# Kernel optimization log

Measured on AMD Instinct MI355X. Metric: run time of the kernel, lower is better.

## Reference

```python
import jax, jax.numpy as jnp
import numpy as np

N, E, ND, ED, HID = 50000, 400000, 128, 64, 128
GIN = 2 * ND + 2  # gnn1 input dim
CIN = 2 * HID + ED  # classifier input dim


def seg_mean(v, idx, n):
    s = jax.ops.segment_sum(v, idx, num_segments=n)
    cnt = jax.ops.segment_sum(jnp.ones((v.shape[0], 1), v.dtype), idx, num_segments=n)
    return s / jnp.maximum(cnt, 1.0)


def layer_norm(h, g, b):
    mu = h.mean(-1, keepdims=True)
    var = ((h - mu) ** 2).mean(-1, keepdims=True)
    return (h - mu) / jnp.sqrt(var + 1e-5) * g + b


def gatv2(h, src, dst, ea, wl, wr, we, att, bias, n, heads):
    # PyG GATv2Conv, concat=False, negative_slope=0.2, add_self_loops with fill_value='mean'
    C = wl.shape[1] // heads
    loop_attr = seg_mean(ea, dst, n)  # self-loop edge_attr = mean of incoming edge_attr
    ar = jnp.arange(n, dtype=src.dtype)
    s = jnp.concatenate([src, ar])
    d = jnp.concatenate([dst, ar])
    ea2 = jnp.concatenate([ea, loop_attr], axis=0)
    xl = (h @ wl).reshape(n, heads, C)
    xr = (h @ wr).reshape(n, heads, C)
    e = xl[s] + xr[d] + (ea2 @ we).reshape(-1, heads, C)  # [E2, H, C]
    e = jax.nn.leaky_relu(e, 0.2)
    logit = (e * att).sum(-1)  # [E2, H]
    m = jax.ops.segment_max(logit, d, num_segments=n)
    m = jnp.where(jnp.isfinite(m), m, 0.0)
    a = jnp.exp(logit - m[d])
    denom = jax.ops.segment_sum(a, d, num_segments=n)
    a = a / jnp.maximum(denom[d], 1e-16)
    out = jax.ops.segment_sum(xl[s] * a[..., None], d, num_segments=n)  # [N, H, C]
    return out.mean(axis=1) + bias


def setup_inputs() -> dict:
    key = jax.random.key(0)
    ks = jax.random.split(key, 32)
    w = lambda k, sh: jax.random.normal(k, sh, jnp.float32) * 0.05
    x = jax.random.normal(ks[0], (N, ND), jnp.float32)
    node_stats = jax.random.uniform(ks[1], (N, 2), jnp.float32)
    src = jax.random.randint(ks[2], (E,), 0, N)
    dst = (src + 1 + jax.random.randint(ks[3], (E,), 0, N - 1)) % N  # guarantees src != dst
    edge_index = jnp.stack([src, dst]).astype(jnp.int32)
    edge_attr = jax.random.normal(ks[4], (E, ED), jnp.float32)
    return {
        'x': x, 'node_stats': node_stats, 'edge_index': edge_index, 'edge_attr': edge_attr,
        'epw': w(ks[5], (ED, ND)), 'epb': jnp.zeros((ND,), jnp.float32),
        'g1wl': w(ks[6], (GIN, 2 * HID)), 'g1wr': w(ks[7], (GIN, 2 * HID)),
        'g1we': w(ks[8], (ED, 2 * HID)), 'g1att': w(ks[9], (2, HID)), 'g1b': jnp.zeros((HID,), jnp.float32),
        'n1g': jnp.ones((HID,), jnp.float32), 'n1b': jnp.zeros((HID,), jnp.float32),
        'g2wl': w(ks[10], (HID, HID)), 'g2wr': w(ks[11], (HID, HID)),
        'g2we': w(ks[12], (ED, HID)), 'g2att': w(ks[13], (1, HID)), 'g2b': jnp.zeros((HID,), jnp.float32),
        'n2g': jnp.ones((HID,), jnp.float32), 'n2b': jnp.zeros((HID,), jnp.float32),
        'c1w': w(ks[14], (CIN, HID)), 'c1b': jnp.zeros((HID,), jnp.float32),
        'c2w': w(ks[15], (HID, HID // 2)), 'c2b': jnp.zeros((HID // 2,), jnp.float32),
        'c3w': w(ks[16], (HID // 2, 1)), 'c3b': jnp.zeros((1,), jnp.float32),
    }


def reference(x, node_stats, edge_index, edge_attr, epw, epb, g1wl, g1wr, g1we, g1att, g1b,
              n1g, n1b, g2wl, g2wr, g2we, g2att, g2b, n2g, n2b, c1w, c1b, c2w, c2b, c3w, c3b):
    src, dst = edge_index[0], edge_index[1]
    n = x.shape[0]
    emb = jax.nn.relu(edge_attr @ epw + epb)  # [E, ND]
    x_out = seg_mean(emb, src, n)
    x_in = seg_mean(emb, dst, n)
    xi = jnp.concatenate([x_out, x_in, node_stats], axis=1)  # [N, GIN]
    h1 = jax.nn.elu(layer_norm(gatv2(xi, src, dst, edge_attr, g1wl, g1wr, g1we, g1att, g1b, n, 2), n1g, n1b))
    h2 = jax.nn.elu(layer_norm(gatv2(h1, src, dst, edge_attr, g2wl, g2wr, g2we, g2att, g2b, n, 1), n2g, n2b))
    er = jnp.concatenate([h2[src], h2[dst], edge_attr], axis=1)  # [E, CIN]
    h = jax.nn.relu(er @ c1w + c1b)
    h = jax.nn.relu(h @ c2w + c2b)
    return h @ c3w + c3b  # [E, 1]
```

## Files before the change

kernel.cpp:

```cpp
#include <hip/hip_runtime.h>
#include <cstdint>
#include <cstddef>


static inline int cdiv(int a, int b) { return (a + b - 1) / b; }

typedef __attribute__((ext_vector_type(8))) short bfrag;
typedef __attribute__((ext_vector_type(4))) float ffrag;

__device__ __forceinline__ float bf2f(unsigned short u) {
  return __uint_as_float(((unsigned)u) << 16);
}
__device__ __forceinline__ unsigned short f2bf(float f) {
  unsigned b = __float_as_uint(f);
  return (unsigned short)((b + 0x7FFFu + ((b >> 16) & 1u)) >> 16);
}

struct PrepJobs {
  const float* src[11];
  unsigned short* dst[11];
  int K[11], Nc[11], KC[11], ld[11];
};
__global__ void prep_bt(PrepJobs J) {
  int j = blockIdx.x;
  int K = J.K[j], Nc = J.Nc[j], KC = J.KC[j], ld = J.ld[j];
  const float* S = J.src[j];
  unsigned short* D = J.dst[j];
  for (int n = blockIdx.y; n < Nc; n += gridDim.y)
    for (int t = threadIdx.x; t < KC; t += blockDim.x) {
      float v = (t < K) ? S[(size_t)t * ld + n] : 0.f;
      D[(size_t)n * KC + t] = f2bf(v);
    }
}

__global__ __launch_bounds__(256) void cvt_bf16(const float* __restrict__ in,
                                                unsigned short* __restrict__ out,
                                                int n4) {
  for (int i = blockIdx.x * blockDim.x + threadIdx.x; i < n4;
       i += gridDim.x * blockDim.x) {
    float4 v = ((const float4*)in)[i];
    ((ushort4*)out)[i] = make_ushort4(f2bf(v.x), f2bf(v.y), f2bf(v.z), f2bf(v.w));
  }
}

__global__ void count_deg(const int* __restrict__ src, const int* __restrict__ dst,
                          int* __restrict__ dsrc, int* __restrict__ ddst, int E) {
  int t = blockIdx.x * blockDim.x + threadIdx.x;
  if (t < E) {
    atomicAdd(&dsrc[src[t]], 1);
    atomicAdd(&ddst[dst[t]], 1);
  }
}

__global__ __launch_bounds__(256) void scan_local(
    const int* __restrict__ degA, const int* __restrict__ degB,
    int* __restrict__ rowA, int* __restrict__ rowB, int* __restrict__ bsum,
    int N, int nb) {
  __shared__ int s[256];
  int arr = blockIdx.y;
  const int* deg = arr ? degB : degA;
  int* row = arr ? rowB : rowA;
  int b = blockIdx.x;
  int i = b * 256 + threadIdx.x;
  int v = (i < N) ? deg[i] : 0;
  s[threadIdx.x] = v;
  __syncthreads();
  for (int off = 1; off < 256; off <<= 1) {
    int t = (threadIdx.x >= off) ? s[threadIdx.x - off] : 0;
    __syncthreads();
    s[threadIdx.x] += t;
    __syncthreads();
  }
  int incl = s[threadIdx.x];
  if (i < N) row[i] = incl - v;
  if (threadIdx.x == 255) bsum[arr * nb + b] = incl;
}

__global__ __launch_bounds__(1024) void scan_bsums(int* __restrict__ bsum, int nb,
                                                   int* __restrict__ rowA,
                                                   int* __restrict__ rowB, int N) {
  __shared__ int s[1024];
  int tid = threadIdx.x;
  for (int arr = 0; arr < 2; arr++) {
    int v = (tid < nb) ? bsum[arr * nb + tid] : 0;
    s[tid] = v;
    __syncthreads();
    for (int off = 1; off < 1024; off <<= 1) {
      int t = (tid >= off) ? s[tid - off] : 0;
      __syncthreads();
      s[tid] += t;
      __syncthreads();
    }
    if (tid < nb) bsum[arr * nb + tid] = s[tid] - v;
    if (tid == nb - 1) {
      int* row = arr ? rowB : rowA;
      row[N] = s[tid];
    }
    __syncthreads();
  }
}

__global__ void scan_add(int* __restrict__ rowA, int* __restrict__ rowB,
                         int* __restrict__ curA, const int* __restrict__ bsum,
                         int N, int nb) {
  int arr = blockIdx.y;
  int* row = arr ? rowB : rowA;
  int b = blockIdx.x;
  int i = b * 256 + threadIdx.x;
  if (i < N) {
    int v = row[i] + bsum[arr * nb + b];
    row[i] = v;
    if (arr == 0) curA[i] = v;
  }
}

__global__ void ext_fix(const int* __restrict__ row_dst, int* __restrict__ row_ext,
                        int* __restrict__ cur_ext, int* __restrict__ ext_eid,
                        int E, int N) {
  int i = blockIdx.x * blockDim.x + threadIdx.x;
  if (i <= N) row_ext[i] = row_dst[i] + i;
  if (i < N) {
    cur_ext[i] = row_dst[i] + i;
    ext_eid[row_dst[i + 1] + i] = E + i;
  }
}

__global__ void scatter_eid(const int* __restrict__ src, const int* __restrict__ dst,
                            int* __restrict__ csrc, int* __restrict__ cext,
                            int* __restrict__ esrc, int* __restrict__ ext_eid,
                            int E) {
  int t = blockIdx.x * blockDim.x + threadIdx.x;
  if (t < E) {
    int p = atomicAdd(&csrc[src[t]], 1);
    esrc[p] = t;
    int q = atomicAdd(&cext[dst[t]], 1);
    ext_eid[q] = t;
  }
}

struct ASrc {
  const float *p0, *p1, *p2;
  int ld0, ld1, ld2, k0, k1;
};
__device__ __forceinline__ float loadA(const ASrc& a, int m, int k) {
  if (k < a.k0) return a.p0[(size_t)m * a.ld0 + k];
  if (k < a.k1) return a.p1[(size_t)m * a.ld1 + (k - a.k0)];
  return a.p2[(size_t)m * a.ld2 + (k - a.k1)];
}
__device__ __forceinline__ int regionOf(const ASrc& a, int k) {
  return k < a.k0 ? 0 : (k < a.k1 ? 1 : 2);
}

template <int ABF>
__device__ __forceinline__ void stageA(
    const ASrc& A, const unsigned short* __restrict__ Abf, int lda,
    unsigned short* asb, int m0, int kc, int M, int K, int tid) {
  int row = tid & 63, kq = tid >> 6;
  int gm = m0 + row;
  if (ABF) {
    const unsigned short* rp = Abf + (size_t)gm * lda + kc + kq * 16;
    ushort4 z = make_ushort4(0, 0, 0, 0);
#pragma unroll
    for (int q = 0; q < 4; q++) {
      ushort4 v = (gm < M) ? *(const ushort4*)(rp + q * 4) : z;
      *(ushort4*)&asb[row * 72 + kq * 16 + q * 4] = v;
    }
  } else {
    bool fastc = (kc + 64 <= K) && (regionOf(A, kc) == regionOf(A, kc + 63)) &&
                 (gm < M);
    if (fastc) {
      int r = regionOf(A, kc);
      const float* p;
      int ld, koff;
      if (r == 0) { p = A.p0; ld = A.ld0; koff = 0; }
      else if (r == 1) { p = A.p1; ld = A.ld1; koff = A.k0; }
      else { p = A.p2; ld = A.ld2; koff = A.k1; }
      const float* rp = p + (size_t)gm * ld + (kc - koff) + kq * 16;
#pragma unroll
      for (int q = 0; q < 4; q++) {
        float4 v = *(const float4*)(rp + q * 4);
        *(ushort4*)&asb[row * 72 + kq * 16 + q * 4] =
            make_ushort4(f2bf(v.x), f2bf(v.y), f2bf(v.z), f2bf(v.w));
      }
    } else {
#pragma unroll
      for (int q = 0; q < 16; q++) {
        int kk = kc + kq * 16 + q;
        float v = (gm < M && kk < K) ? loadA(A, gm, kk) : 0.f;
        asb[row * 72 + kq * 16 + q] = f2bf(v);
      }
    }
  }
}

template <int ACT, int OBF, int ABF>
__global__ __launch_bounds__(256) void gemm_mfma(
    ASrc A, const unsigned short* __restrict__ Abf, int lda,
    const unsigned short* __restrict__ Bt, int ldbt,
    const float* __restrict__ bias, void* __restrict__ Cv, int ldc, int M, int K) {
  __shared__ __align__(16) unsigned short asb[64 * 72];
  __shared__ __align__(16) unsigned short bsb[128 * 72];
  int tid = threadIdx.x;
  int m0 = blockIdx.x * 64, n0 = blockIdx.y * 128;
  int lane = tid & 63, wave = tid >> 6;
  int quad = lane >> 4, l16 = lane & 15;
  ffrag zero = {0.f, 0.f, 0.f, 0.f};
  ffrag acc[8];
#pragma unroll
  for (int t = 0; t < 8; t++) acc[t] = zero;
  int KC = (K + 63) & ~63;
  for (int kc = 0; kc < KC; kc += 64) {
    __syncthreads();
    stageA<ABF>(A, Abf, lda, asb, m0, kc, M, K, tid);
    {
      int n = tid >> 1, hf = tid & 1;
      const ushort4* rp = (const ushort4*)(Bt + (size_t)(n0 + n) * ldbt + kc + hf * 32);
      ushort4* dp = (ushort4*)&bsb[n * 72 + hf * 32];
#pragma unroll
      for (int i = 0; i < 8; i++) dp[i] = rp[i];
    }
    __syncthreads();
    int arow = wave * 16 + l16;
    bfrag a0 = *(const bfrag*)&asb[arow * 72 + quad * 8];
    bfrag a1 = *(const bfrag*)&asb[arow * 72 + 32 + quad * 8];
#pragma unroll
    for (int t = 0; t < 8; t++) {
      int bn = t * 16 + l16;
      bfrag b0 = *(const bfrag*)&bsb[bn * 72 + quad * 8];
      bfrag b1 = *(const bfrag*)&bsb[bn * 72 + 32 + quad * 8];
      acc[t] = __builtin_amdgcn_mfma_f32_16x16x32_bf16(a0, b0, acc[t], 0, 0, 0);
      acc[t] = __builtin_amdgcn_mfma_f32_16x16x32_bf16(a1, b1, acc[t], 0, 0, 0);
    }
  }
#pragma unroll
  for (int t = 0; t < 8; t++) {
    int col = n0 + t * 16 + l16;
    float bv = bias ? bias[col] : 0.f;
#pragma unroll
    for (int r = 0; r < 4; r++) {
      int row = m0 + wave * 16 + quad * 4 + r;
      if (row < M) {
        float v = acc[t][r] + bv;
        if (ACT == 1) v = fmaxf(v, 0.f);
        if (OBF)
          ((unsigned short*)Cv)[(size_t)row * ldc + col] = f2bf(v);
        else
          ((float*)Cv)[(size_t)row * ldc + col] = v;
      }
    }
  }
}

template <int OBF, int ABF>
__global__ __launch_bounds__(256) void gemm_dual(
    ASrc A, const unsigned short* __restrict__ Abf, int lda,
    const unsigned short* __restrict__ Bt1, const unsigned short* __restrict__ Bt2,
    int ldbt, void* __restrict__ Cv1, void* __restrict__ Cv2, int ldc,
    int M, int K) {
  __shared__ __align__(16) unsigned short asb[64 * 72];
  __shared__ __align__(16) unsigned short bsb[128 * 72];
  int tid = threadIdx.x;
  int m0 = blockIdx.x * 64, n0 = blockIdx.y * 128;
  int lane = tid & 63, wave = tid >> 6;
  int quad = lane >> 4, l16 = lane & 15;
  ffrag zero = {0.f, 0.f, 0.f, 0.f};
  ffrag acc1[8], acc2[8];
#pragma unroll
  for (int t = 0; t < 8; t++) { acc1[t] = zero; acc2[t] = zero; }
  int KC = (K + 63) & ~63;
  int arow = wave * 16 + l16;
  for (int kc = 0; kc < KC; kc += 64) {
    __syncthreads();
    stageA<ABF>(A, Abf, lda, asb, m0, kc, M, K, tid);
    {
      int n = tid >> 1, hf = tid & 1;
      const ushort4* rp = (const ushort4*)(Bt1 + (size_t)(n0 + n) * ldbt + kc + hf * 32);
      ushort4* dp = (ushort4*)&bsb[n * 72 + hf * 32];
#pragma unroll
      for (int i = 0; i < 8; i++) dp[i] = rp[i];
    }
    __syncthreads();
    bfrag a0 = *(const bfrag*)&asb[arow * 72 + quad * 8];
    bfrag a1 = *(const bfrag*)&asb[arow * 72 + 32 + quad * 8];
#pragma unroll
    for (int t = 0; t < 8; t++) {
      int bn = t * 16 + l16;
      bfrag b0 = *(const bfrag*)&bsb[bn * 72 + quad * 8];
      bfrag b1 = *(const bfrag*)&bsb[bn * 72 + 32 + quad * 8];
      acc1[t] = __builtin_amdgcn_mfma_f32_16x16x32_bf16(a0, b0, acc1[t], 0, 0, 0);
      acc1[t] = __builtin_amdgcn_mfma_f32_16x16x32_bf16(a1, b1, acc1[t], 0, 0, 0);
    }
    __syncthreads();
    {
      int n = tid >> 1, hf = tid & 1;
      const ushort4* rp = (const ushort4*)(Bt2 + (size_t)(n0 + n) * ldbt + kc + hf * 32);
      ushort4* dp = (ushort4*)&bsb[n * 72 + hf * 32];
#pragma unroll
      for (int i = 0; i < 8; i++) dp[i] = rp[i];
    }
    __syncthreads();
#pragma unroll
    for (int t = 0; t < 8; t++) {
      int bn = t * 16 + l16;
      bfrag b0 = *(const bfrag*)&bsb[bn * 72 + quad * 8];
      bfrag b1 = *(const bfrag*)&bsb[bn * 72 + 32 + quad * 8];
      acc2[t] = __builtin_amdgcn_mfma_f32_16x16x32_bf16(a0, b0, acc2[t], 0, 0, 0);
      acc2[t] = __builtin_amdgcn_mfma_f32_16x16x32_bf16(a1, b1, acc2[t], 0, 0, 0);
    }
  }
#pragma unroll
  for (int t = 0; t < 8; t++) {
    int col = n0 + t * 16 + l16;
#pragma unroll
    for (int r = 0; r < 4; r++) {
      int row = m0 + wave * 16 + quad * 4 + r;
      if (row < M) {
        if (OBF) {
          ((unsigned short*)Cv1)[(size_t)row * ldc + col] = f2bf(acc1[t][r]);
          ((unsigned short*)Cv2)[(size_t)row * ldc + col] = f2bf(acc2[t][r]);
        } else {
          ((float*)Cv1)[(size_t)row * ldc + col] = acc1[t][r];
          ((float*)Cv2)[(size_t)row * ldc + col] = acc2[t][r];
        }
      }
    }
  }
}

__global__ __launch_bounds__(256) void gather_mean(
    const int* __restrict__ row_src, const int* __restrict__ eid_src,
    const int* __restrict__ row_ext, const int* __restrict__ ext_eid,
    const unsigned short* __restrict__ emb, const unsigned short* __restrict__ eab,
    float* __restrict__ xout, float* __restrict__ xin,
    unsigned short* __restrict__ lattrb, int N) {
  int lane = threadIdx.x & 63, wid = threadIdx.x >> 6;
  int n = blockIdx.x * 4 + wid;
  int side = blockIdx.y;
  if (n >= N) return;
  int lo, hi;
  const int* eid;
  if (side) { lo = row_ext[n]; hi = row_ext[n + 1] - 1; eid = ext_eid; }
  else { lo = row_src[n]; hi = row_src[n + 1]; eid = eid_src; }
  float a0 = 0.f, a1 = 0.f, la = 0.f;
  for (int j = lo; j < hi; j++) {
    int e = eid[j];
    ushort2 v = *(const ushort2*)&emb[(size_t)e * 128 + lane * 2];
    a0 += bf2f(v.x);
    a1 += bf2f(v.y);
    if (side) la += bf2f(eab[(size_t)e * 64 + lane]);
  }
  float r = 1.f / fmaxf((float)(hi - lo), 1.f);
  float* ob = side ? xin : xout;
  *(float2*)&ob[(size_t)n * 128 + lane * 2] = make_float2(a0 * r, a1 * r);
  if (side) lattrb[(size_t)n * 64 + lane] = f2bf(la * r);
}

template <int H>
__global__ __launch_bounds__(256) void attn_logits_mfma(
    const unsigned short* __restrict__ xl, const unsigned short* __restrict__ xr,
    const int* __restrict__ src, const int* __restrict__ dst,
    const unsigned short* __restrict__ eab, const unsigned short* __restrict__ lattrb,
    const int* __restrict__ ext_eid,
    const unsigned short* __restrict__ wet, const float* __restrict__ att,
    float* __restrict__ lg, int E, int N) {
  constexpr int HC = H * 128;
  __shared__ __align__(16) unsigned short asb[64 * 72];
  __shared__ __align__(16) unsigned short bsb[128 * 72];
  __shared__ float atts[128];
  __shared__ int sidx[64], didx[64];
  unsigned short* Cs = bsb;
  int tid = threadIdx.x;
  int E2 = E + N;
  int i0 = blockIdx.x * 64;
  int lane = tid & 63, wave = tid >> 6, quad = lane >> 4, l16 = lane & 15;
  if (tid < 64) {
    int j = i0 + tid;
    int s = 0, d = 0;
    if (j < E2) {
      int e = ext_eid[j];
      if (e < E) { s = src[e]; d = dst[e]; }
      else { s = d = e - E; }
    }
    sidx[tid] = s;
    didx[tid] = d;
  }
  {
    int row = tid & 63, kq = tid >> 6;
    int j = i0 + row;
    if (j < E2) {
      int e = ext_eid[j];
      const unsigned short* ap =
          (e < E) ? eab + (size_t)e * 64 : lattrb + (size_t)(e - E) * 64;
      const ushort4* rp = (const ushort4*)(ap + kq * 16);
#pragma unroll
      for (int q = 0; q < 4; q++)
        *(ushort4*)&asb[row * 72 + kq * 16 + q * 4] = rp[q];
    } else {
      ushort4 z = make_ushort4(0, 0, 0, 0);
#pragma unroll
      for (int q = 0; q < 4; q++) *(ushort4*)&asb[row * 72 + kq * 16 + q * 4] = z;
    }
  }
  int er = tid >> 4, cc = tid & 15;
  ffrag zero = {0.f, 0.f, 0.f, 0.f};
  for (int head = 0; head < H; head++) {
    int n0 = head * 128;
    __syncthreads();
    if (tid < 128) atts[tid] = att[n0 + tid];
    {
      int n = tid >> 1, hf = tid & 1;
      const ushort4* rp = (const ushort4*)(wet + (size_t)(n0 + n) * 64 + hf * 32);
      ushort4* dp = (ushort4*)&bsb[n * 72 + hf * 32];
#pragma unroll
      for (int i = 0; i < 8; i++) dp[i] = rp[i];
    }
    __syncthreads();
    int arow = wave * 16 + l16;
    bfrag a0 = *(const bfrag*)&asb[arow * 72 + quad * 8];
    bfrag a1 = *(const bfrag*)&asb[arow * 72 + 32 + quad * 8];
    ffrag acc[8];
#pragma unroll
    for (int t = 0; t < 8; t++) {
      acc[t] = zero;
      int bn = t * 16 + l16;
      bfrag b0 = *(const bfrag*)&bsb[bn * 72 + quad * 8];
      bfrag b1 = *(const bfrag*)&bsb[bn * 72 + 32 + quad * 8];
      acc[t] = __builtin_amdgcn_mfma_f32_16x16x32_bf16(a0, b0, acc[t], 0, 0, 0);
      acc[t] = __builtin_amdgcn_mfma_f32_16x16x32_bf16(a1, b1, acc[t], 0, 0, 0);
    }
    __syncthreads();
    {
      int rb = wave * 16 + quad * 4;
#pragma unroll
      for (int t = 0; t < 8; t++)
#pragma unroll
        for (int r = 0; r < 4; r++)
          Cs[(rb + r) * 136 + t * 16 + l16] = f2bf(acc[t][r]);
    }
    __syncthreads();
#pragma unroll
    for (int i2 = 0; i2 < 4; i2++) {
      int r = er * 4 + i2;
      int gi = i0 + r;
      float ps = 0.f;
      if (gi < E2) {
        int s = sidx[r], d = didx[r];
#pragma unroll
        for (int h = 0; h < 2; h++) {
          int c = h * 64 + cc * 4;
          ushort4 mv = *(const ushort4*)&Cs[r * 136 + c];
          ushort4 xlu = *(const ushort4*)&xl[(size_t)s * HC + n0 + c];
          ushort4 xru = *(const ushort4*)&xr[(size_t)d * HC + n0 + c];
          float e0 = bf2f(mv.x) + bf2f(xlu.x) + bf2f(xru.x);
          float e1 = bf2f(mv.y) + bf2f(xlu.y) + bf2f(xru.y);
          float e2 = bf2f(mv.z) + bf2f(xlu.z) + bf2f(xru.z);
          float e3 = bf2f(mv.w) + bf2f(xlu.w) + bf2f(xru.w);
          e0 = e0 > 0.f ? e0 : 0.2f * e0;
          e1 = e1 > 0.f ? e1 : 0.2f * e1;
          e2 = e2 > 0.f ? e2 : 0.2f * e2;
          e3 = e3 > 0.f ? e3 : 0.2f * e3;
          ps += e0 * atts[c + 0] + e1 * atts[c + 1] + e2 * atts[c + 2] +
                e3 * atts[c + 3];
        }
      }
      ps += __shfl_xor(ps, 1);
      ps += __shfl_xor(ps, 2);
      ps += __shfl_xor(ps, 4);
      ps += __shfl_xor(ps, 8);
      if (cc == 0 && gi < E2) lg[(size_t)gi * H + head] = ps;
    }
  }
}

template <int H>
__global__ __launch_bounds__(256) void attn_fused(
    const unsigned short* __restrict__ xl, const float* __restrict__ lg,
    const int* __restrict__ row_ext, const int* __restrict__ ext_eid,
    const int* __restrict__ src, const float* __restrict__ bias,
    const float* __restrict__ gam, const float* __restrict__ bet,
    unsigned short* __restrict__ hout, int E, int N) {
  constexpr int HC = H * 128;
  constexpr int CPL = HC / 64;
  int lane = threadIdx.x & 63, wid = threadIdx.x >> 6;
  int n = blockIdx.x * 4 + wid;
  if (n >= N) return;
  int lo = row_ext[n], hi = row_ext[n + 1];
  int myh = (H == 2) ? (lane >> 5) : 0;
  int colbase = (H == 2) ? (myh * 128 + (lane & 31) * 4) : (lane * 2);
  float m = -3.4e38f;
  for (int j = lo; j < hi; j++) m = fmaxf(m, lg[(size_t)j * H + myh]);
  float asum = 0.f;
  float acc[CPL] = {};
  for (int j = lo; j < hi; j++) {
    int e = ext_eid[j];
    int s = (e < E) ? src[e] : (e - E);
    float a = __expf(lg[(size_t)j * H + myh] - m);
    asum += a;
    const unsigned short* xp = &xl[(size_t)s * HC + colbase];
    if (H == 2) {
      ushort4 u = *(const ushort4*)xp;
      acc[0] += a * bf2f(u.x);
      acc[1] += a * bf2f(u.y);
      acc[2] += a * bf2f(u.z);
      acc[3] += a * bf2f(u.w);
    } else {
      ushort2 u = *(const ushort2*)xp;
      acc[0] += a * bf2f(u.x);
      acc[1] += a * bf2f(u.y);
    }
  }
  float inv = 1.f / fmaxf(asum, 1e-16f);
#pragma unroll
  for (int k = 0; k < CPL; k++) acc[k] *= inv;
  int ch;
  if (H == 2) {
#pragma unroll
    for (int k = 0; k < CPL; k++) acc[k] = (acc[k] + __shfl_xor(acc[k], 32)) * 0.5f;
    ch = (lane & 31) * CPL;
  } else {
    ch = lane * CPL;
  }
#pragma unroll
  for (int k = 0; k < CPL; k++) acc[k] += bias[ch + k];
  float s = 0.f;
#pragma unroll
  for (int k = 0; k < CPL; k++) s += acc[k];
#pragma unroll
  for (int mm = 1; mm < 64; mm <<= 1) s += __shfl_xor(s, mm);
  constexpr float dupn = (H == 2) ? 256.f : 128.f;
  float mu = s / dupn;
  float vs = 0.f;
#pragma unroll
  for (int k = 0; k < CPL; k++) {
    acc[k] -= mu;
    vs += acc[k] * acc[k];
  }
#pragma unroll
  for (int mm = 1; mm < 64; mm <<= 1) vs += __shfl_xor(vs, mm);
  float rstd = rsqrtf(vs / dupn + 1e-5f);
  float y[CPL];
#pragma unroll
  for (int k = 0; k < CPL; k++) {
    float v = acc[k] * rstd * gam[ch + k] + bet[ch + k];
    y[k] = v > 0.f ? v : expm1f(v);
  }
  if (H == 2) {
    if (lane < 32)
      *(ushort4*)&hout[(size_t)n * 128 + ch] =
          make_ushort4(f2bf(y[0]), f2bf(y[1]), f2bf(y[2]), f2bf(y[3]));
  } else {
    *(ushort2*)&hout[(size_t)n * 128 + ch] = make_ushort2(f2bf(y[0]), f2bf(y[1]));
  }
}

__global__ __launch_bounds__(256) void classifier_mfma(
    const unsigned short* __restrict__ eab, const unsigned short* __restrict__ Wct,
    const int* __restrict__ eid_src,
    const int* __restrict__ src, const int* __restrict__ dst,
    const float* __restrict__ P, const float* __restrict__ Q,
    const float* __restrict__ c1b, const unsigned short* __restrict__ c2t,
    const float* __restrict__ c2b, const float* __restrict__ c3w,
    const float* __restrict__ c3b, float* __restrict__ out, int E) {
  __shared__ __align__(16) unsigned short asb[64 * 72];
  __shared__ __align__(16) unsigned short bsb[128 * 72];
  __shared__ __align__(16) unsigned short t1s[64 * 136];
  __shared__ float c1bs[128];
  __shared__ float c2bs[64], c3ws[64];
  __shared__ int sidx[64], didx[64], eidx[64];
  int tid = threadIdx.x;
  int e0 = blockIdx.x * 64;
  int lane = tid & 63, wave = tid >> 6, quad = lane >> 4, l16 = lane & 15;
  if (tid < 128) c1bs[tid] = c1b[tid];
  if (tid < 64) {
    c2bs[tid] = c2b[tid];
    c3ws[tid] = c3w[tid];
    int j = e0 + tid;
    int e = (j < E) ? eid_src[j] : 0;
    eidx[tid] = (j < E) ? e : -1;
    sidx[tid] = src[e];
    didx[tid] = dst[e];
  }
  {
    int row = tid & 63, kq = tid >> 6;
    int j = e0 + row;
    if (j < E) {
      int e = eid_src[j];
      const ushort4* rp = (const ushort4*)(eab + (size_t)e * 64 + kq * 16);
#pragma unroll
      for (int q = 0; q < 4; q++)
        *(ushort4*)&asb[row * 72 + kq * 16 + q * 4] = rp[q];
    } else {
      ushort4 z = make_ushort4(0, 0, 0, 0);
#pragma unroll
      for (int q = 0; q < 4; q++) *(ushort4*)&asb[row * 72 + kq * 16 + q * 4] = z;
    }
  }
  {
    int n = tid >> 1, hf = tid & 1;
    const ushort4* rp = (const ushort4*)(Wct + (size_t)n * 64 + hf * 32);
    ushort4* dp = (ushort4*)&bsb[n * 72 + hf * 32];
#pragma unroll
    for (int i = 0; i < 8; i++) dp[i] = rp[i];
  }
  __syncthreads();
  ffrag zero = {0.f, 0.f, 0.f, 0.f};
  int arow = wave * 16 + l16;
  {
    bfrag a0 = *(const bfrag*)&asb[arow * 72 + quad * 8];
    bfrag a1 = *(const bfrag*)&asb[arow * 72 + 32 + quad * 8];
    ffrag acc[8];
#pragma unroll
    for (int t = 0; t < 8; t++) {
      acc[t] = zero;
      int bn = t * 16 + l16;
      bfrag b0 = *(const bfrag*)&bsb[bn * 72 + quad * 8];
      bfrag b1 = *(const bfrag*)&bsb[bn * 72 + 32 + quad * 8];
      acc[t] = __builtin_amdgcn_mfma_f32_16x16x32_bf16(a0, b0, acc[t], 0, 0, 0);
      acc[t] = __builtin_amdgcn_mfma_f32_16x16x32_bf16(a1, b1, acc[t], 0, 0, 0);
    }
    __syncthreads();
    int rb = wave * 16 + quad * 4;
#pragma unroll
    for (int t = 0; t < 8; t++)
#pragma unroll
      for (int r = 0; r < 4; r++)
        t1s[(rb + r) * 136 + t * 16 + l16] = f2bf(acc[t][r]);
  }
  __syncthreads();
  {
    int erow = tid >> 4, ccc = tid & 15;
#pragma unroll
    for (int i2 = 0; i2 < 4; i2++) {
      int r = erow * 4 + i2;
      int s = sidx[r], d = didx[r];
#pragma unroll
      for (int h = 0; h < 2; h++) {
        int c = h * 64 + ccc * 4;
        ushort4 mv = *(const ushort4*)&t1s[r * 136 + c];
        float4 pv = *(const float4*)&P[(size_t)s * 128 + c];
        float4 qv = *(const float4*)&Q[(size_t)d * 128 + c];
        float v0 = fmaxf(bf2f(mv.x) + pv.x + qv.x + c1bs[c + 0], 0.f);
        float v1 = fmaxf(bf2f(mv.y) + pv.y + qv.y + c1bs[c + 1], 0.f);
        float v2 = fmaxf(bf2f(mv.z) + pv.z + qv.z + c1bs[c + 2], 0.f);
        float v3 = fmaxf(bf2f(mv.w) + pv.w + qv.w + c1bs[c + 3], 0.f);
        *(ushort4*)&t1s[r * 136 + c] =
            make_ushort4(f2bf(v0), f2bf(v1), f2bf(v2), f2bf(v3));
      }
    }
    int n = tid >> 2, qq = tid & 3;
    const ushort4* rp = (const ushort4*)(c2t + (size_t)n * 128 + qq * 32);
    ushort4* dp = (ushort4*)&bsb[n * 136 + qq * 32];
#pragma unroll
    for (int i = 0; i < 8; i++) dp[i] = rp[i];
  }
  __syncthreads();
  {
    bfrag pa[4];
#pragma unroll
    for (int kc = 0; kc < 4; kc++)
      pa[kc] = *(const bfrag*)&t1s[arow * 136 + kc * 32 + quad * 8];
    ffrag acc2[4];
#pragma unroll
    for (int t = 0; t < 4; t++) {
      acc2[t] = zero;
      int bn = t * 16 + l16;
#pragma unroll
      for (int kc = 0; kc < 4; kc++) {
        bfrag b = *(const bfrag*)&bsb[bn * 136 + kc * 32 + quad * 8];
        acc2[t] = __builtin_amdgcn_mfma_f32_16x16x32_bf16(pa[kc], b, acc2[t], 0, 0, 0);
      }
    }
    float c3b0 = c3b[0];
    float rsum[4] = {0.f, 0.f, 0.f, 0.f};
#pragma unroll
    for (int t = 0; t < 4; t++) {
      int col = t * 16 + l16;
      float cb = c2bs[col], cw = c3ws[col];
#pragma unroll
      for (int r = 0; r < 4; r++)
        rsum[r] += fmaxf(acc2[t][r] + cb, 0.f) * cw;
    }
#pragma unroll
    for (int r = 0; r < 4; r++) {
      rsum[r] += __shfl_xor(rsum[r], 1);
      rsum[r] += __shfl_xor(rsum[r], 2);
      rsum[r] += __shfl_xor(rsum[r], 4);
      rsum[r] += __shfl_xor(rsum[r], 8);
    }
    if (l16 == 0) {
#pragma unroll
      for (int r = 0; r < 4; r++) {
        int e = eidx[wave * 16 + quad * 4 + r];
        if (e >= 0) out[e] = rsum[r] + c3b0;
      }
    }
  }
}

extern "C" void kernel_launch(void* const* d_in, const int* in_sizes, int n_in,
                              void* d_out, int out_size, void* d_ws, size_t ws_size,
                              hipStream_t stream) {
  const int N = in_sizes[1] / 2;
  const int E = in_sizes[3] / 64;
  const int E2 = E + N;
  const int nb = cdiv(N, 256);

  const float* node_stats = (const float*)d_in[1];
  const int* src = (const int*)d_in[2];
  const int* dst = (const int*)d_in[2] + E;
  const float* edge_attr = (const float*)d_in[3];
  const float* epw = (const float*)d_in[4];
  const float* epb = (const float*)d_in[5];
  const float* g1wl = (const float*)d_in[6];
  const float* g1wr = (const float*)d_in[7];
  const float* g1we = (const float*)d_in[8];
  const float* g1att = (const float*)d_in[9];
  const float* g1b = (const float*)d_in[10];
  const float* n1g = (const float*)d_in[11];
  const float* n1b = (const float*)d_in[12];
  const float* g2wl = (const float*)d_in[13];
  const float* g2wr = (const float*)d_in[14];
  const float* g2we = (const float*)d_in[15];
  const float* g2att = (const float*)d_in[16];
  const float* g2b = (const float*)d_in[17];
  const float* n2g = (const float*)d_in[18];
  const float* n2b = (const float*)d_in[19];
  const float* c1w = (const float*)d_in[20];
  const float* c1b = (const float*)d_in[21];
  const float* c2w = (const float*)d_in[22];
  const float* c2b = (const float*)d_in[23];
  const float* c3w = (const float*)d_in[24];
  const float* c3b = (const float*)d_in[25];
  float* out = (float*)d_out;

  float* w = (float*)d_ws;
  size_t o = 0;
  auto alloc = [&](size_t n) { float* p = w + o; o += n; return p; };
  float* xout = alloc((size_t)N * 128);
  float* xin = alloc((size_t)N * 128);
  float* lattr = alloc((size_t)N * 64);
  float* lg = alloc((size_t)E2 * 2);
  int* row_src = (int*)alloc((size_t)(N + 1));
  int* row_dst = (int*)alloc((size_t)(N + 1));
  int* row_ext = (int*)alloc((size_t)(N + 1));
  int* deg_src = (int*)alloc((size_t)N);
  int* deg_dst = (int*)alloc((size_t)N);
  int* cur_src = (int*)alloc((size_t)N);
  int* cur_ext = (int*)alloc((size_t)N);
  int* eid_src = (int*)alloc((size_t)E);
  int* ext_eid = (int*)alloc((size_t)E2);
  int* bsum = (int*)alloc((size_t)2 * 1024);
  unsigned short* wb = (unsigned short*)alloc(140000);
  unsigned short* eab = (unsigned short*)alloc((size_t)E * 32);
  float* R = alloc((size_t)E * 64);
  unsigned short* Ru = (unsigned short*)R;
  unsigned short* emb = Ru;
  unsigned short* xl1b = Ru;
  unsigned short* xr1b = Ru + (size_t)N * 256;
  unsigned short* h1b = Ru + (size_t)N * 512;
  unsigned short* xl2b = Ru + (size_t)N * 640;
  unsigned short* xr2b = Ru + (size_t)N * 768;
  unsigned short* h2b = Ru + (size_t)N * 896;
  unsigned short* lattrb = (unsigned short*)lattr;
  float* P = xout;
  float* Q = xin;

  unsigned short* epwt = wb + 0;
  unsigned short* g1wlt = wb + 8192;
  unsigned short* g1wrt = wb + 90112;
  unsigned short* g1wet = wb + 172032;
  unsigned short* g2wlt = wb + 188416;
  unsigned short* g2wrt = wb + 204800;
  unsigned short* g2wet = wb + 221184;
  unsigned short* c1wat = wb + 229376;
  unsigned short* c1wbt = wb + 245760;
  unsigned short* c1wct = wb + 262144;
  unsigned short* c2t = wb + 270336;

  cvt_bf16<<<2048, 256, 0, stream>>>(edge_attr, eab, E * 16);
  PrepJobs J;
  auto setj = [&](int i, const float* s, unsigned short* d2, int K, int Nc,
                  int KC, int ld) {
    J.src[i] = s; J.dst[i] = d2; J.K[i] = K; J.Nc[i] = Nc; J.KC[i] = KC; J.ld[i] = ld;
  };
  setj(0, epw, epwt, 64, 128, 64, 128);
  setj(1, g1wl, g1wlt, 258, 256, 320, 256);
  setj(2, g1wr, g1wrt, 258, 256, 320, 256);
  setj(3, g1we, g1wet, 64, 256, 64, 256);
  setj(4, g2wl, g2wlt, 128, 128, 128, 128);
  setj(5, g2wr, g2wrt, 128, 128, 128, 128);
  setj(6, g2we, g2wet, 64, 128, 64, 128);
  setj(7, c1w, c1wat, 128, 128, 128, 128);
  setj(8, c1w + 128 * 128, c1wbt, 128, 128, 128, 128);
  setj(9, c1w + 256 * 128, c1wct, 64, 128, 64, 128);
  setj(10, c2w, c2t, 128, 64, 128, 64);
  prep_bt<<<dim3(11, 32), 256, 0, stream>>>(J);

  hipMemsetAsync(deg_src, 0, (size_t)2 * N * sizeof(int), stream);
  count_deg<<<cdiv(E, 256), 256, 0, stream>>>(src, dst, deg_src, deg_dst, E);
  scan_local<<<dim3(nb, 2), 256, 0, stream>>>(deg_src, deg_dst, row_src, row_dst,
                                              bsum, N, nb);
  scan_bsums<<<1, 1024, 0, stream>>>(bsum, nb, row_src, row_dst, N);
  scan_add<<<dim3(nb, 2), 256, 0, stream>>>(row_src, row_dst, cur_src, bsum, N, nb);
  ext_fix<<<cdiv(N + 1, 256), 256, 0, stream>>>(row_dst, row_ext, cur_ext,
                                                ext_eid, E, N);
  scatter_eid<<<cdiv(E, 256), 256, 0, stream>>>(src, dst, cur_src, cur_ext,
                                                eid_src, ext_eid, E);

  ASrc dummy{nullptr, nullptr, nullptr, 0, 0, 0, 0, 0};

  gemm_mfma<1, 1, 1><<<dim3(cdiv(E, 64), 1), 256, 0, stream>>>(
      dummy, eab, 64, epwt, 64, epb, emb, 128, E, 64);
  gather_mean<<<dim3(cdiv(N, 4), 2), 256, 0, stream>>>(
      row_src, eid_src, row_ext, ext_eid, emb, eab, xout, xin, lattrb, N);

  {
    ASrc a{xout, xin, node_stats, 128, 128, 2, 128, 256};
    dim3 g(cdiv(N, 64), 2);
    gemm_dual<1, 0><<<g, 256, 0, stream>>>(a, nullptr, 0, g1wlt, g1wrt, 320,
                                           xl1b, xr1b, 256, N, 258);
  }

  attn_logits_mfma<2><<<cdiv(E2, 64), 256, 0, stream>>>(
      xl1b, xr1b, src, dst, eab, lattrb, ext_eid, g1wet, g1att, lg, E, N);
  attn_fused<2><<<cdiv(N, 4), 256, 0, stream>>>(xl1b, lg, row_ext, ext_eid, src,
                                                g1b, n1g, n1b, h1b, E, N);

  {
    dim3 g(cdiv(N, 64), 1);
    gemm_dual<1, 1><<<g, 256, 0, stream>>>(dummy, h1b, 128, g2wlt, g2wrt, 128,
                                           xl2b, xr2b, 128, N, 128);
  }

  attn_logits_mfma<1><<<cdiv(E2, 64), 256, 0, stream>>>(
      xl2b, xr2b, src, dst, eab, lattrb, ext_eid, g2wet, g2att, lg, E, N);
  attn_fused<1><<<cdiv(N, 4), 256, 0, stream>>>(xl2b, lg, row_ext, ext_eid, src,
                                                g2b, n2g, n2b, h2b, E, N);

  {
    dim3 g(cdiv(N, 64), 1);
    gemm_dual<0, 1><<<g, 256, 0, stream>>>(dummy, h2b, 128, c1wat, c1wbt, 128,
                                           P, Q, 128, N, 128);
  }
  classifier_mfma<<<cdiv(E, 64), 256, 0, stream>>>(
      eab, c1wct, eid_src, src, dst, P, Q, c1b, c2t, c2b, c3w, c3b, out, E);
}
```

Before: 988.6 us.

## Fuse GATv2 softmax aggregation into logits kernel with atomic scatter

The attention logits kernel now exponentiates each logit directly, with a clamp instead of subtracting the per-node max, and accumulates weighted xl rows and denominators into per-destination fp32 buffers with atomics. Consecutive edges that share a destination are merged in registers before flushing. A light finalize kernel then normalizes, averages heads and applies layernorm and ELU. This drops the logits buffer round-trip and the second CSR gather pass over xl, at the cost of float atomics, memsets, nondeterministic summation and possible overflow or accuracy loss without max subtraction.

```diff
diff --git a/kernel.cpp b/kernel.cpp
--- a/kernel.cpp
+++ b/kernel.cpp
@@ -362,7 +362,7 @@
     const unsigned short* __restrict__ eab, const unsigned short* __restrict__ lattrb,
     const int* __restrict__ ext_eid,
     const unsigned short* __restrict__ wet, const float* __restrict__ att,
-    float* __restrict__ lg, int E, int N) {
+    float* __restrict__ acc_g, float* __restrict__ den_g, int E, int N) {
   constexpr int HC = H * 128;
   __shared__ __align__(16) unsigned short asb[64 * 72];
   __shared__ __align__(16) unsigned short bsb[128 * 72];
@@ -375,7 +375,7 @@
   int lane = tid & 63, wave = tid >> 6, quad = lane >> 4, l16 = lane & 15;
   if (tid < 64) {
     int j = i0 + tid;
-    int s = 0, d = 0;
+    int s = 0, d = -1;
     if (j < E2) {
       int e = ext_eid[j];
       if (e < E) { s = src[e]; d = dst[e]; }
@@ -438,119 +438,115 @@
           Cs[(rb + r) * 136 + t * 16 + l16] = f2bf(acc[t][r]);
     }
     __syncthreads();
-#pragma unroll
-    for (int i2 = 0; i2 < 4; i2++) {
-      int r = er * 4 + i2;
-      int gi = i0 + r;
-      float ps = 0.f;
-      if (gi < E2) {
-        int s = sidx[r], d = didx[r];
-#pragma unroll
-        for (int h = 0; h < 2; h++) {
-          int c = h * 64 + cc * 4;
-          ushort4 mv = *(const ushort4*)&Cs[r * 136 + c];
-          ushort4 xlu = *(const ushort4*)&xl[(size_t)s * HC + n0 + c];
-          ushort4 xru = *(const ushort4*)&xr[(size_t)d * HC + n0 + c];
-          float e0 = bf2f(mv.x) + bf2f(xlu.x) + bf2f(xru.x);
-          float e1 = bf2f(mv.y) + bf2f(xlu.y) + bf2f(xru.y);
-          float e2 = bf2f(mv.z) + bf2f(xlu.z) + bf2f(xru.z);
-          float e3 = bf2f(mv.w) + bf2f(xlu.w) + bf2f(xru.w);
-          e0 = e0 > 0.f ? e0 : 0.2f * e0;
-          e1 = e1 > 0.f ? e1 : 0.2f * e1;
-          e2 = e2 > 0.f ? e2 : 0.2f * e2;
-          e3 = e3 > 0.f ? e3 : 0.2f * e3;
-          ps += e0 * atts[c + 0] + e1 * atts[c + 1] + e2 * atts[c + 2] +
-                e3 * atts[c + 3];
+    {
+      float racc[8] = {0.f, 0.f, 0.f, 0.f, 0.f, 0.f, 0.f, 0.f};
+      float rden = 0.f;
+      int cur = -1;
+#pragma unroll
+      for (int i2 = 0; i2 < 4; i2++) {
+        int r = er * 4 + i2;
+        int d = didx[r];
+        if (d != cur) {
+          if (cur >= 0) {
+            float* ap = acc_g + (size_t)cur * HC + n0;
+#pragma unroll
+            for (int h = 0; h < 2; h++)
+#pragma unroll
+              for (int q = 0; q < 4; q++)
+                atomicAdd(&ap[h * 64 + cc * 4 + q], racc[h * 4 + q]);
+            if (cc == 0) atomicAdd(&den_g[(size_t)cur * H + head], rden);
+#pragma unroll
+            for (int k = 0; k < 8; k++) racc[k] = 0.f;
+            rden = 0.f;
+          }
+          cur = d;
+        }
+        if (d >= 0) {
+          int s = sidx[r];
+          float xv[8];
+          float ps = 0.f;
+#pragma unroll
+          for (int h = 0; h < 2; h++) {
+            int c = h * 64 + cc * 4;
+            ushort4 mv = *(const ushort4*)&Cs[r * 136 + c];
+            ushort4 xlu = *(const ushort4*)&xl[(size_t)s * HC + n0 + c];
+            ushort4 xru = *(const ushort4*)&xr[(size_t)d * HC + n0 + c];
+            float x0 = bf2f(xlu.x), x1 = bf2f(xlu.y), x2 = bf2f(xlu.z),
+                  x3 = bf2f(xlu.w);
+            xv[h * 4 + 0] = x0;
+            xv[h * 4 + 1] = x1;
+            xv[h * 4 + 2] = x2;
+            xv[h * 4 + 3] = x3;
+            float e0 = bf2f(mv.x) + x0 + bf2f(xru.x);
+            float e1 = bf2f(mv.y) + x1 + bf2f(xru.y);
+            float e2 = bf2f(mv.z) + x2 + bf2f(xru.z);
+            float e3 = bf2f(mv.w) + x3 + bf2f(xru.w);
+            e0 = e0 > 0.f ? e0 : 0.2f * e0;
+            e1 = e1 > 0.f ? e1 : 0.2f * e1;
+            e2 = e2 > 0.f ? e2 : 0.2f * e2;
+            e3 = e3 > 0.f ? e3 : 0.2f * e3;
+            ps += e0 * atts[c + 0] + e1 * atts[c + 1] + e2 * atts[c + 2] +
+                  e3 * atts[c + 3];
+          }
+          ps += __shfl_xor(ps, 1);
+          ps += __shfl_xor(ps, 2);
+          ps += __shfl_xor(ps, 4);
+          ps += __shfl_xor(ps, 8);
+          float a = __expf(fminf(ps, 60.f));
+          rden += a;
+#pragma unroll
+          for (int k = 0; k < 8; k++) racc[k] += a * xv[k];
         }
       }
-      ps += __shfl_xor(ps, 1);
-      ps += __shfl_xor(ps, 2);
-      ps += __shfl_xor(ps, 4);
-      ps += __shfl_xor(ps, 8);
-      if (cc == 0 && gi < E2) lg[(size_t)gi * H + head] = ps;
+      if (cur >= 0) {
+        float* ap = acc_g + (size_t)cur * HC + n0;
+#pragma unroll
+        for (int h = 0; h < 2; h++)
+#pragma unroll
+          for (int q = 0; q < 4; q++)
+            atomicAdd(&ap[h * 64 + cc * 4 + q], racc[h * 4 + q]);
+        if (cc == 0) atomicAdd(&den_g[(size_t)cur * H + head], rden);
+      }
     }
   }
 }
 
 template <int H>
-__global__ __launch_bounds__(256) void attn_fused(
-    const unsigned short* __restrict__ xl, const float* __restrict__ lg,
-    const int* __restrict__ row_ext, const int* __restrict__ ext_eid,
-    const int* __restrict__ src, const float* __restrict__ bias,
-    const float* __restrict__ gam, const float* __restrict__ bet,
-    unsigned short* __restrict__ hout, int E, int N) {
-  constexpr int HC = H * 128;
-  constexpr int CPL = HC / 64;
+__global__ __launch_bounds__(256) void attn_finalize(
+    const float* __restrict__ acc, const float* __restrict__ den,
+    const float* __restrict__ bias, const float* __restrict__ gam,
+    const float* __restrict__ bet, unsigned short* __restrict__ hout, int N) {
   int lane = threadIdx.x & 63, wid = threadIdx.x >> 6;
   int n = blockIdx.x * 4 + wid;
   if (n >= N) return;
-  int lo = row_ext[n], hi = row_ext[n + 1];
-  int myh = (H == 2) ? (lane >> 5) : 0;
-  int colbase = (H == 2) ? (myh * 128 + (lane & 31) * 4) : (lane * 2);
-  float m = -3.4e38f;
-  for (int j = lo; j < hi; j++) m = fmaxf(m, lg[(size_t)j * H + myh]);
-  float asum = 0.f;
-  float acc[CPL] = {};
-  for (int j = lo; j < hi; j++) {
-    int e = ext_eid[j];
-    int s = (e < E) ? src[e] : (e - E);
-    float a = __expf(lg[(size_t)j * H + myh] - m);
-    asum += a;
-    const unsigned short* xp = &xl[(size_t)s * HC + colbase];
-    if (H == 2) {
-      ushort4 u = *(const ushort4*)xp;
-      acc[0] += a * bf2f(u.x);
-      acc[1] += a * bf2f(u.y);
-      acc[2] += a * bf2f(u.z);
-      acc[3] += a * bf2f(u.w);
-    } else {
-      ushort2 u = *(const ushort2*)xp;
-      acc[0] += a * bf2f(u.x);
-      acc[1] += a * bf2f(u.y);
-    }
-  }
-  float inv = 1.f / fmaxf(asum, 1e-16f);
-#pragma unroll
-  for (int k = 0; k < CPL; k++) acc[k] *= inv;
-  int ch;
+  int c = lane * 2;
+  float v0, v1;
   if (H == 2) {
-#pragma unroll
-    for (int k = 0; k < CPL; k++) acc[k] = (acc[k] + __shfl_xor(acc[k], 32)) * 0.5f;
-    ch = (lane & 31) * CPL;
+    const float* ar = acc + (size_t)n * 256;
+    float i0 = 1.f / fmaxf(den[(size_t)n * 2 + 0], 1e-16f);
+    float i1 = 1.f / fmaxf(den[(size_t)n * 2 + 1], 1e-16f);
+    v0 = 0.5f * (ar[c] * i0 + ar[128 + c] * i1) + bias[c];
+    v1 = 0.5f * (ar[c + 1] * i0 + ar[128 + c + 1] * i1) + bias[c + 1];
   } else {
-    ch = lane * CPL;
-  }
-#pragma unroll
-  for (int k = 0; k < CPL; k++) acc[k] += bias[ch + k];
-  float s = 0.f;
-#pragma unroll
-  for (int k = 0; k < CPL; k++) s += acc[k];
+    const float* ar = acc + (size_t)n * 128;
+    float i0 = 1.f / fmaxf(den[n], 1e-16f);
+    v0 = ar[c] * i0 + bias[c];
+    v1 = ar[c + 1] * i0 + bias[c + 1];
+  }
+  float s = v0 + v1;
 #pragma unroll
   for (int mm = 1; mm < 64; mm <<= 1) s += __shfl_xor(s, mm);
-  constexpr float dupn = (H == 2) ? 256.f : 128.f;
-  float mu = s / dupn;
-  float vs = 0.f;
-#pragma unroll
-  for (int k = 0; k < CPL; k++) {
-    acc[k] -= mu;
-    vs += acc[k] * acc[k];
-  }
+  float mu = s * (1.f / 128.f);
+  float a0 = v0 - mu, a1 = v1 - mu;
+  float vs = a0 * a0 + a1 * a1;
 #pragma unroll
   for (int mm = 1; mm < 64; mm <<= 1) vs += __shfl_xor(vs, mm);
-  float rstd = rsqrtf(vs / dupn + 1e-5f);
-  float y[CPL];
-#pragma unroll
-  for (int k = 0; k < CPL; k++) {
-    float v = acc[k] * rstd * gam[ch + k] + bet[ch + k];
-    y[k] = v > 0.f ? v : expm1f(v);
-  }
-  if (H == 2) {
-    if (lane < 32)
-      *(ushort4*)&hout[(size_t)n * 128 + ch] =
-          make_ushort4(f2bf(y[0]), f2bf(y[1]), f2bf(y[2]), f2bf(y[3]));
-  } else {
-    *(ushort2*)&hout[(size_t)n * 128 + ch] = make_ushort2(f2bf(y[0]), f2bf(y[1]));
-  }
+  float rstd = rsqrtf(vs * (1.f / 128.f) + 1e-5f);
+  float y0 = a0 * rstd * gam[c] + bet[c];
+  float y1 = a1 * rstd * gam[c + 1] + bet[c + 1];
+  y0 = y0 > 0.f ? y0 : expm1f(y0);
+  y1 = y1 > 0.f ? y1 : expm1f(y1);
+  *(ushort2*)&hout[(size_t)n * 128 + c] = make_ushort2(f2bf(y0), f2bf(y1));
 }
 
 __global__ __launch_bounds__(256) void classifier_mfma(
@@ -739,7 +735,6 @@
   float* xout = alloc((size_t)N * 128);
   float* xin = alloc((size_t)N * 128);
   float* lattr = alloc((size_t)N * 64);
-  float* lg = alloc((size_t)E2 * 2);
   int* row_src = (int*)alloc((size_t)(N + 1));
   int* row_dst = (int*)alloc((size_t)(N + 1));
   int* row_ext = (int*)alloc((size_t)(N + 1));
@@ -762,6 +757,10 @@
   unsigned short* xr2b = Ru + (size_t)N * 768;
   unsigned short* h2b = Ru + (size_t)N * 896;
   unsigned short* lattrb = (unsigned short*)lattr;
+  float* den1 = lattr + (size_t)N * 32;
+  float* den2 = den1 + (size_t)N * 2;
+  float* acc1 = xout;
+  float* acc2 = xout;
   float* P = xout;
   float* Q = xin;
 
@@ -821,10 +820,12 @@
                                            xl1b, xr1b, 256, N, 258);
   }
 
+  hipMemsetAsync(acc1, 0, (size_t)N * 256 * sizeof(float), stream);
+  hipMemsetAsync(den1, 0, (size_t)N * 3 * sizeof(float), stream);
   attn_logits_mfma<2><<<cdiv(E2, 64), 256, 0, stream>>>(
-      xl1b, xr1b, src, dst, eab, lattrb, ext_eid, g1wet, g1att, lg, E, N);
-  attn_fused<2><<<cdiv(N, 4), 256, 0, stream>>>(xl1b, lg, row_ext, ext_eid, src,
-                                                g1b, n1g, n1b, h1b, E, N);
+      xl1b, xr1b, src, dst, eab, lattrb, ext_eid, g1wet, g1att, acc1, den1, E, N);
+  attn_finalize<2><<<cdiv(N, 4), 256, 0, stream>>>(acc1, den1, g1b, n1g, n1b,
+                                                   h1b, N);
 
   {
     dim3 g(cdiv(N, 64), 1);
@@ -832,10 +833,11 @@
                                            xl2b, xr2b, 128, N, 128);
   }
 
+  hipMemsetAsync(acc2, 0, (size_t)N * 128 * sizeof(float), stream);
   attn_logits_mfma<1><<<cdiv(E2, 64), 256, 0, stream>>>(
-      xl2b, xr2b, src, dst, eab, lattrb, ext_eid, g2wet, g2att, lg, E, N);
-  attn_fused<1><<<cdiv(N, 4), 256, 0, stream>>>(xl2b, lg, row_ext, ext_eid, src,
-                                                g2b, n2g, n2b, h2b, E, N);
+      xl2b, xr2b, src, dst, eab, lattrb, ext_eid, g2wet, g2att, acc2, den2, E, N);
+  attn_finalize<1><<<cdiv(N, 4), 256, 0, stream>>>(acc2, den2, g2b, n2g, n2b,
+                                                   h2b, N);
 
   {
     dim3 g(cdiv(N, 64), 1);
```

Result: slower. 1.556 ms (+57.4%).
